# Kernel tuning notes

Hardware: AMD Instinct MI355X
Metric: run time of the kernel (lower is better)

The kernel has to match this reference:

```python
import jax, jax.numpy as jnp
import numpy as np

M, N, NNZ, NITER = 1_000_000, 1_000_000, 8_000_000, 5


def setup_inputs() -> dict:
    key = jax.random.key(0)
    ks = jax.random.split(key, 24)
    f32 = jnp.float32
    inp = dict(
        rows=jax.random.randint(ks[0], (NNZ,), 0, M, dtype=jnp.int32),
        cols=jax.random.randint(ks[1], (NNZ,), 0, N, dtype=jnp.int32),
        vals=jax.random.normal(ks[2], (NNZ,), dtype=f32) * 0.1,
        b=jax.random.normal(ks[3], (M, 1), dtype=f32),
        c=jax.random.normal(ks[4], (N, 1), dtype=f32),
        solution=jax.random.normal(ks[5], (N, 1), dtype=f32),
        dual_solution=jax.random.normal(ks[6], (M, 1), dtype=f32),
        x0=jax.random.normal(ks[7], (N, 1), dtype=f32),  # beta=1 init
        y0=jax.random.normal(ks[8], (M, 1), dtype=f32),  # std_y=1 init
        # dual tower: Conv1d(10->4), Conv1d(6->4), update Conv1d(6->1)
        dw1=jax.random.normal(ks[9], (4, 10), dtype=f32) * 0.3,
        db1=jax.random.normal(ks[10], (4,), dtype=f32) * 0.1,
        dw2=jax.random.normal(ks[11], (4, 6), dtype=f32) * 0.3,
        db2=jax.random.normal(ks[12], (4,), dtype=f32) * 0.1,
        dwu=jax.random.normal(ks[13], (1, 6), dtype=f32) * 0.1,
        dbu=jax.random.normal(ks[14], (1,), dtype=f32) * 0.1,
        # primal tower: Conv1d(10->4), Conv1d(6->4), update Conv1d(6->1)
        pw1=jax.random.normal(ks[15], (4, 10), dtype=f32) * 0.3,
        pb1=jax.random.normal(ks[16], (4,), dtype=f32) * 0.1,
        pw2=jax.random.normal(ks[17], (4, 6), dtype=f32) * 0.3,
        pb2=jax.random.normal(ks[18], (4,), dtype=f32) * 0.1,
        pwu=jax.random.normal(ks[19], (1, 6), dtype=f32) * 0.1,
        pbu=jax.random.normal(ks[20], (1,), dtype=f32) * 0.1,
        nb_max_iter=NITER,
    )
    return inp


def reference(rows, cols, vals, b, c, solution, dual_solution, x0, y0,
              dw1, db1, dw2, db2, dwu, dbu,
              pw1, pb1, pw2, pb2, pwu, pbu, nb_max_iter):
    m, n = b.shape[0], c.shape[0]

    def A_mm(X):   # sparse A @ X : [n,k] -> [m,k]
        return jax.ops.segment_sum(vals[:, None] * X[cols], rows, num_segments=m)

    def At_mm(Y):  # sparse A.T @ Y : [m,k] -> [n,k]
        return jax.ops.segment_sum(vals[:, None] * Y[rows], cols, num_segments=n)

    def step(carry, _):
        x, y, x_h, y_h = carry  # x[n,1] y[m,1] x_h[4,n] y_h[4,m]
        # dual update
        r = A_mm(x) - b                                   # [m,1]
        atxh = A_mm(x_h.T)                                # [m,4]
        h = jnp.concatenate([y_h, atxh.T, y.T, r.T], 0)   # [10,m]
        h = jax.nn.relu(dw1 @ h + db1[:, None])           # [4,m]
        h = jnp.concatenate([h, y.T, r.T], 0)             # [6,m]
        y_h = jax.nn.relu(dw2 @ h + db2[:, None])         # [4,m]
        h2 = jnp.concatenate([y_h, y.T, r.T], 0)          # [6,m]
        y = y + (dwu @ h2 + dbu[:, None]).T               # [m,1]
        # primal update
        d = c + At_mm(y)                                  # [n,1]
        atyh = At_mm(y_h.T)                               # [n,4]
        g = jnp.concatenate([x_h, atyh.T, x.T, d.T], 0)   # [10,n]
        g = jax.nn.relu(pw1 @ g + pb1[:, None])           # [4,n]
        g = jnp.concatenate([g, x.T, d.T], 0)             # [6,n]
        x_h = jax.nn.relu(pw2 @ g + pb2[:, None])         # [4,n]
        g2 = jnp.concatenate([x_h, x.T, d.T], 0)          # [6,n]
        x = x + (pwu @ g2 + pbu[:, None]).T               # [n,1]
        dp = jnp.sqrt(jnp.sum((x - solution) ** 2))
        dd = jnp.sqrt(jnp.sum((y - dual_solution) ** 2))
        return (x, y, x_h, y_h), (dp, dd)

    init = (x0, y0,
            jnp.zeros((4, n), dtype=x0.dtype),
            jnp.zeros((4, m), dtype=y0.dtype))
    (x, y, _, _), (dps, dds) = jax.lax.scan(step, init, None, length=nb_max_iter)

    loss_primal = jnp.mean(dps) + 1.0 * jnp.mean(jax.nn.relu(dps[1:] - dps[:-1]))
    loss_dual = jnp.mean(dds) + 1.0 * jnp.mean(jax.nn.relu(dds[1:] - dds[:-1]))
    loss = loss_primal + loss_dual
    return x, y, loss, dps, dds
```

## Files before the change

kernel.cpp:

```cpp
#include <hip/hip_runtime.h>
#include <math.h>


#define NITER 5
#define NBK_SHIFT 9
#define NBK (1 << NBK_SHIFT)
#define NBK_MAX 2048
#define CH 16384
#define SORT_CAP 6144

__device__ __forceinline__ float blockReduceSum(float v) {
#pragma unroll
  for (int off = 32; off > 0; off >>= 1) v += __shfl_down(v, off, 64);
  __shared__ float smem[8];
  const int lane = threadIdx.x & 63;
  const int wid = threadIdx.x >> 6;
  if (lane == 0) smem[wid] = v;
  __syncthreads();
  float r = 0.f;
  if (threadIdx.x == 0) {
    const int nw = (blockDim.x + 63) >> 6;
    for (int w = 0; w < nw; ++w) r += smem[w];
  }
  return r;
}

__global__ __launch_bounds__(1024) void zero_meta(int* __restrict__ cntA,
                                                  int* __restrict__ cntT,
                                                  float* __restrict__ red) {
  const int i = threadIdx.x;
  cntA[i] = 0;
  cntA[i + 1024] = 0;
  cntT[i] = 0;
  cntT[i + 1024] = 0;
  if (i < 16) red[i] = 0.f;
}

__global__ __launch_bounds__(256) void hist2(const int* __restrict__ rows,
                                             const int* __restrict__ cols,
                                             int* __restrict__ cntA,
                                             int* __restrict__ cntT, int nnz) {
  __shared__ int hA[NBK_MAX];
  __shared__ int hT[NBK_MAX];
  for (int i = threadIdx.x; i < NBK_MAX; i += 256) { hA[i] = 0; hT[i] = 0; }
  __syncthreads();
  const int stride = gridDim.x * blockDim.x;
  for (int e = blockIdx.x * blockDim.x + threadIdx.x; e < nnz; e += stride) {
    atomicAdd(&hA[rows[e] >> NBK_SHIFT], 1);
    atomicAdd(&hT[cols[e] >> NBK_SHIFT], 1);
  }
  __syncthreads();
  for (int i = threadIdx.x; i < NBK_MAX; i += 256) {
    if (hA[i]) atomicAdd(&cntA[i], hA[i]);
    if (hT[i]) atomicAdd(&cntT[i], hT[i]);
  }
}

__global__ __launch_bounds__(1024) void scan_bases(const int* __restrict__ cnt,
                                                   int* __restrict__ base,
                                                   int* __restrict__ fill,
                                                   int nb) {
  __shared__ int sm[1024];
  int run = 0;
  for (int s = 0; s < nb; s += 1024) {
    const int i = s + threadIdx.x;
    const int x = (i < nb) ? cnt[i] : 0;
    sm[threadIdx.x] = x;
    __syncthreads();
#pragma unroll
    for (int off = 1; off < 1024; off <<= 1) {
      const int add = (threadIdx.x >= off) ? sm[threadIdx.x - off] : 0;
      __syncthreads();
      sm[threadIdx.x] += add;
      __syncthreads();
    }
    if (i < nb) {
      const int ex = run + sm[threadIdx.x] - x;
      base[i] = ex;
      fill[i] = ex;
    }
    const int tot = sm[1023];
    __syncthreads();
    run += tot;
  }
}

__global__ __launch_bounds__(512) void scatter2(
    const int* __restrict__ rows, const int* __restrict__ cols,
    const float* __restrict__ vals, int* __restrict__ fillA,
    int* __restrict__ fillT, int2* __restrict__ eA, int2* __restrict__ eT,
    int nnz) {
  __shared__ int hA[NBK_MAX];
  __shared__ int hT[NBK_MAX];
  for (int i = threadIdx.x; i < NBK_MAX; i += 512) { hA[i] = 0; hT[i] = 0; }
  __syncthreads();
  const int e0 = blockIdx.x * CH;
  for (int k = threadIdx.x; k < CH; k += 512) {
    const int e = e0 + k;
    if (e < nnz) {
      atomicAdd(&hA[rows[e] >> NBK_SHIFT], 1);
      atomicAdd(&hT[cols[e] >> NBK_SHIFT], 1);
    }
  }
  __syncthreads();
  for (int i = threadIdx.x; i < NBK_MAX; i += 512) {
    const int cA = hA[i];
    if (cA) hA[i] = atomicAdd(&fillA[i], cA);
    const int cT = hT[i];
    if (cT) hT[i] = atomicAdd(&fillT[i], cT);
  }
  __syncthreads();
  for (int k = threadIdx.x; k < CH; k += 512) {
    const int e = e0 + k;
    if (e < nnz) {
      const int r = rows[e];
      const int c = cols[e];
      const int vb = __float_as_int(vals[e]);
      const int pA = atomicAdd(&hA[r >> NBK_SHIFT], 1);
      eA[pA] = make_int2(((r & (NBK - 1)) << 20) | c, vb);
      const int pT = atomicAdd(&hT[c >> NBK_SHIFT], 1);
      eT[pT] = make_int2(((c & (NBK - 1)) << 20) | r, vb);
    }
  }
}

__global__ __launch_bounds__(512) void sort_bucket(const int* __restrict__ base,
                                                   const int* __restrict__ cnt,
                                                   int2* __restrict__ edges) {
  __shared__ int2 recs[SORT_CAP];
  __shared__ int hist[NBK];
  const int bkt = blockIdx.x;
  const int beg = base[bkt];
  const int num = cnt[bkt];
  if (num > SORT_CAP) return;
  if (threadIdx.x < NBK) hist[threadIdx.x] = 0;
  __syncthreads();
  for (int k = threadIdx.x; k < num; k += 512) {
    const int2 r = edges[beg + k];
    recs[k] = r;
    atomicAdd(&hist[((unsigned)r.x) >> 20], 1);
  }
  __syncthreads();
  int x = 0, incl = 0;
  if (threadIdx.x < NBK) { x = hist[threadIdx.x]; incl = x; }
#pragma unroll
  for (int off = 1; off < NBK; off <<= 1) {
    int add = 0;
    if (threadIdx.x < NBK && threadIdx.x >= off) add = hist[threadIdx.x - off];
    __syncthreads();
    if (threadIdx.x < NBK) {
      incl += add;
      hist[threadIdx.x] = incl;
    }
    __syncthreads();
  }
  if (threadIdx.x < NBK) hist[threadIdx.x] = incl - x;
  __syncthreads();
  for (int k = threadIdx.x; k < num; k += 512) {
    const int2 r = recs[k];
    const int p = atomicAdd(&hist[((unsigned)r.x) >> 20], 1);
    edges[beg + p] = r;
  }
}

__global__ __launch_bounds__(256) void init_state2(const float* __restrict__ x0,
                                                   const float* __restrict__ y0,
                                                   float* __restrict__ X5,
                                                   float* __restrict__ Y5,
                                                   int n, int m) {
  const int i = blockIdx.x * blockDim.x + threadIdx.x;
  if (i < n) {
    float* xp = X5 + (size_t)i * 8;
    xp[0] = x0[i];
    xp[1] = 0.f; xp[2] = 0.f; xp[3] = 0.f; xp[4] = 0.f;
  }
  if (i < m) {
    float* yp = Y5 + (size_t)i * 8;
    yp[0] = y0[i];
    yp[1] = 0.f; yp[2] = 0.f; yp[3] = 0.f; yp[4] = 0.f;
  }
}

__global__ __launch_bounds__(256) void fused_bucket_tower(
    const int* __restrict__ base, const int* __restrict__ cnt,
    const int2* __restrict__ edges, const float* __restrict__ src,
    float* __restrict__ state, const float* __restrict__ seed, float sign,
    const float* __restrict__ sol, const float* __restrict__ w1,
    const float* __restrict__ b1, const float* __restrict__ w2,
    const float* __restrict__ b2, const float* __restrict__ wu,
    const float* __restrict__ bu, float* __restrict__ red_slot, int count) {
  __shared__ float acc[NBK * 5];
  for (int i = threadIdx.x; i < NBK * 5; i += 256) acc[i] = 0.f;
  __syncthreads();
  const int bkt = blockIdx.x;
  const int beg = base[bkt];
  const int num = cnt[bkt];
  const int lane = threadIdx.x & 63;
  for (int k0 = 0; k0 < num; k0 += 512) {
    const int kA = k0 + threadIdx.x;
    const int kB = k0 + 256 + threadIdx.x;
    int dlA = -1, dlB = -1;
    float vA = 0.f, vB = 0.f;
    float4 loA = make_float4(0.f, 0.f, 0.f, 0.f);
    float4 loB = make_float4(0.f, 0.f, 0.f, 0.f);
    float s4A = 0.f, s4B = 0.f;
    if (kA < num) {
      const int2 ed = edges[beg + kA];
      dlA = ((unsigned)ed.x) >> 20;
      vA = __int_as_float(ed.y);
      const float* sp = src + (size_t)(ed.x & 0xFFFFF) * 8;
      loA = *reinterpret_cast<const float4*>(sp);
      s4A = sp[4];
    }
    if (kB < num) {
      const int2 ed = edges[beg + kB];
      dlB = ((unsigned)ed.x) >> 20;
      vB = __int_as_float(ed.y);
      const float* sp = src + (size_t)(ed.x & 0xFFFFF) * 8;
      loB = *reinterpret_cast<const float4*>(sp);
      s4B = sp[4];
    }
    {
      float m0 = vA * loA.x, m1 = vA * loA.y, m2 = vA * loA.z,
            m3 = vA * loA.w, m4 = vA * s4A;
      int dl = dlA;
#pragma unroll
      for (int off = 1; off < 64; off <<= 1) {
        const int dlu = __shfl_up(dl, off, 64);
        const float t0 = __shfl_up(m0, off, 64);
        const float t1 = __shfl_up(m1, off, 64);
        const float t2 = __shfl_up(m2, off, 64);
        const float t3 = __shfl_up(m3, off, 64);
        const float t4 = __shfl_up(m4, off, 64);
        if (lane >= off && dlu == dl) {
          m0 += t0; m1 += t1; m2 += t2; m3 += t3; m4 += t4;
        }
      }
      const int dld = __shfl_down(dl, 1, 64);
      if (dl >= 0 && ((lane == 63) || (dld != dl))) {
        float* ap = acc + dl * 5;
        atomicAdd(ap + 0, m0);
        atomicAdd(ap + 1, m1);
        atomicAdd(ap + 2, m2);
        atomicAdd(ap + 3, m3);
        atomicAdd(ap + 4, m4);
      }
    }
    {
      float m0 = vB * loB.x, m1 = vB * loB.y, m2 = vB * loB.z,
            m3 = vB * loB.w, m4 = vB * s4B;
      int dl = dlB;
#pragma unroll
      for (int off = 1; off < 64; off <<= 1) {
        const int dlu = __shfl_up(dl, off, 64);
        const float t0 = __shfl_up(m0, off, 64);
        const float t1 = __shfl_up(m1, off, 64);
        const float t2 = __shfl_up(m2, off, 64);
        const float t3 = __shfl_up(m3, off, 64);
        const float t4 = __shfl_up(m4, off, 64);
        if (lane >= off && dlu == dl) {
          m0 += t0; m1 += t1; m2 += t2; m3 += t3; m4 += t4;
        }
      }
      const int dld = __shfl_down(dl, 1, 64);
      if (dl >= 0 && ((lane == 63) || (dld != dl))) {
        float* ap = acc + dl * 5;
        atomicAdd(ap + 0, m0);
        atomicAdd(ap + 1, m1);
        atomicAdd(ap + 2, m2);
        atomicAdd(ap + 3, m3);
        atomicAdd(ap + 4, m4);
      }
    }
  }
  __syncthreads();
  float part = 0.f;
  for (int t = threadIdx.x; t < NBK; t += 256) {
    const int row = (bkt << NBK_SHIFT) + t;
    if (row < count) {
      const float* a = acc + t * 5;
      const float r = a[0] + sign * seed[row];
      float* sp = state + (size_t)row * 8;
      const float4 st = *reinterpret_cast<const float4*>(sp);
      const float y = st.x;
      float v[10];
      v[0] = st.y; v[1] = st.z; v[2] = st.w; v[3] = sp[4];
      v[4] = a[1]; v[5] = a[2]; v[6] = a[3]; v[7] = a[4];
      v[8] = y;
      v[9] = r;
      float h[4];
#pragma unroll
      for (int o = 0; o < 4; ++o) {
        float accv = b1[o];
#pragma unroll
        for (int kk = 0; kk < 10; ++kk) accv += w1[o * 10 + kk] * v[kk];
        h[o] = fmaxf(accv, 0.f);
      }
      float hn[4];
#pragma unroll
      for (int o = 0; o < 4; ++o) {
        float accv = b2[o] + w2[o * 6 + 4] * y + w2[o * 6 + 5] * r;
#pragma unroll
        for (int kk = 0; kk < 4; ++kk) accv += w2[o * 6 + kk] * h[kk];
        hn[o] = fmaxf(accv, 0.f);
      }
      const float upd = bu[0] + wu[0] * hn[0] + wu[1] * hn[1] + wu[2] * hn[2] +
                        wu[3] * hn[3] + wu[4] * y + wu[5] * r;
      const float yn = y + upd;
      float4 stn;
      stn.x = yn; stn.y = hn[0]; stn.z = hn[1]; stn.w = hn[2];
      *reinterpret_cast<float4*>(sp) = stn;
      sp[4] = hn[3];
      const float diff = yn - sol[row];
      part += diff * diff;
    }
  }
  const float bs = blockReduceSum(part);
  if (threadIdx.x == 0) unsafeAtomicAdd(red_slot, bs);
}

__global__ __launch_bounds__(256) void finalize2(const float* __restrict__ X5,
                                                 const float* __restrict__ Y5,
                                                 const float* __restrict__ red,
                                                 float* __restrict__ out, int n,
                                                 int m) {
  const int i = blockIdx.x * blockDim.x + threadIdx.x;
  if (i < n) out[i] = X5[(size_t)i * 8];
  if (i < m) out[n + i] = Y5[(size_t)i * 8];
  if (i == 0) {
    float dps[NITER], dds[NITER];
#pragma unroll
    for (int t = 0; t < NITER; ++t) {
      dps[t] = sqrtf(red[t]);
      dds[t] = sqrtf(red[NITER + t]);
    }
    float mp = 0.f, md = 0.f, rp = 0.f, rd = 0.f;
#pragma unroll
    for (int t = 0; t < NITER; ++t) { mp += dps[t]; md += dds[t]; }
#pragma unroll
    for (int t = 1; t < NITER; ++t) {
      rp += fmaxf(dps[t] - dps[t - 1], 0.f);
      rd += fmaxf(dds[t] - dds[t - 1], 0.f);
    }
    out[n + m] = mp / NITER + rp / (NITER - 1) + md / NITER + rd / (NITER - 1);
#pragma unroll
    for (int t = 0; t < NITER; ++t) {
      out[n + m + 1 + t] = dps[t];
      out[n + m + 1 + NITER + t] = dds[t];
    }
  }
}

template <int S>
__global__ __launch_bounds__(256) void init_state(
    const float* __restrict__ x0, const float* __restrict__ y0,
    const float* __restrict__ b, float* __restrict__ X5,
    float* __restrict__ Y5, float* __restrict__ Yacc, float* __restrict__ red,
    int n, int m) {
  const int i = blockIdx.x * blockDim.x + threadIdx.x;
  if (i < 16) red[i] = 0.f;
  if (i < n) {
    float* xp = X5 + (size_t)i * S;
    xp[0] = x0[i];
    xp[1] = 0.f; xp[2] = 0.f; xp[3] = 0.f; xp[4] = 0.f;
  }
  if (i < m) {
    float* yp = Y5 + (size_t)i * S;
    yp[0] = y0[i];
    yp[1] = 0.f; yp[2] = 0.f; yp[3] = 0.f; yp[4] = 0.f;
    float* ya = Yacc + (size_t)i * S;
    ya[0] = -b[i];
    ya[1] = 0.f; ya[2] = 0.f; ya[3] = 0.f; ya[4] = 0.f;
  }
}

template <int S>
__global__ __launch_bounds__(256) void spmm5(const int* __restrict__ gidx,
                                             const int* __restrict__ sidx,
                                             const float* __restrict__ vals,
                                             const float* __restrict__ src,
                                             float* __restrict__ dst, int nnz) {
  const int e = blockIdx.x * blockDim.x + threadIdx.x;
  if (e >= nnz) return;
  const int g = gidx[e];
  const int s = sidx[e];
  const float v = vals[e];
  const float* sp = src + (size_t)g * S;
  float s0, s1, s2, s3, s4;
  if constexpr (S == 8) {
    const float4 lo = *reinterpret_cast<const float4*>(sp);
    s0 = lo.x; s1 = lo.y; s2 = lo.z; s3 = lo.w; s4 = sp[4];
  } else {
    s0 = sp[0]; s1 = sp[1]; s2 = sp[2]; s3 = sp[3]; s4 = sp[4];
  }
  float* dp = dst + (size_t)s * S;
  unsafeAtomicAdd(dp + 0, v * s0);
  unsafeAtomicAdd(dp + 1, v * s1);
  unsafeAtomicAdd(dp + 2, v * s2);
  unsafeAtomicAdd(dp + 3, v * s3);
  unsafeAtomicAdd(dp + 4, v * s4);
}

template <int S>
__global__ __launch_bounds__(256) void tower(
    const float* __restrict__ acc, float* __restrict__ state,
    const float* __restrict__ prep_src, float* __restrict__ prep_dst,
    float sign, const float* __restrict__ sol, const float* __restrict__ w1,
    const float* __restrict__ b1, const float* __restrict__ w2,
    const float* __restrict__ b2, const float* __restrict__ wu,
    const float* __restrict__ bu, float* __restrict__ red_slot, int count,
    int prep_count) {
  const int i = blockIdx.x * blockDim.x + threadIdx.x;
  float part = 0.f;
  if (i < count) {
    const float* a = acc + (size_t)i * S;
    const float r = a[0];
    float* sp = state + (size_t)i * S;
    const float y = sp[0];
    float v[10];
    v[0] = sp[1]; v[1] = sp[2]; v[2] = sp[3]; v[3] = sp[4];
    v[4] = a[1];  v[5] = a[2];  v[6] = a[3];  v[7] = a[4];
    v[8] = y;
    v[9] = r;
    float h[4];
#pragma unroll
    for (int o = 0; o < 4; ++o) {
      float accv = b1[o];
#pragma unroll
      for (int k = 0; k < 10; ++k) accv += w1[o * 10 + k] * v[k];
      h[o] = fmaxf(accv, 0.f);
    }
    float hn[4];
#pragma unroll
    for (int o = 0; o < 4; ++o) {
      float accv = b2[o] + w2[o * 6 + 4] * y + w2[o * 6 + 5] * r;
#pragma unroll
      for (int k = 0; k < 4; ++k) accv += w2[o * 6 + k] * h[k];
      hn[o] = fmaxf(accv, 0.f);
    }
    const float upd = bu[0] + wu[0] * hn[0] + wu[1] * hn[1] + wu[2] * hn[2] +
                      wu[3] * hn[3] + wu[4] * y + wu[5] * r;
    const float yn = y + upd;
    sp[0] = yn;
    sp[1] = hn[0]; sp[2] = hn[1]; sp[3] = hn[2]; sp[4] = hn[3];
    const float diff = yn - sol[i];
    part = diff * diff;
  }
  if (i < prep_count) {
    float* pd = prep_dst + (size_t)i * S;
    pd[0] = sign * prep_src[i];
    pd[1] = 0.f; pd[2] = 0.f; pd[3] = 0.f; pd[4] = 0.f;
  }
  const float bs = blockReduceSum(part);
  if (threadIdx.x == 0) unsafeAtomicAdd(red_slot, bs);
}

template <int S>
static void run_atomic(const int* rows, const int* cols, const float* vals,
                       const float* b, const float* c, const float* solution,
                       const float* dual_solution, const float* x0,
                       const float* y0, const float* dw1, const float* db1,
                       const float* dw2, const float* db2, const float* dwu,
                       const float* dbu, const float* pw1, const float* pb1,
                       const float* pw2, const float* pb2, const float* pwu,
                       const float* pbu, float* out, float* ws, int n, int m,
                       int nnz, hipStream_t stream) {
  float* X5 = ws;
  float* Y5 = X5 + (size_t)n * S;
  float* Xacc = Y5 + (size_t)m * S;
  float* Yacc = Xacc + (size_t)n * S;
  float* red = Yacc + (size_t)m * S;

  const int BLK = 256;
  const int nm = (n > m) ? n : m;
  const int gN = (nm + BLK - 1) / BLK;
  const int gE = (nnz + BLK - 1) / BLK;

  init_state<S><<<gN, BLK, 0, stream>>>(x0, y0, b, X5, Y5, Yacc, red, n, m);
  for (int t = 0; t < NITER; ++t) {
    spmm5<S><<<gE, BLK, 0, stream>>>(cols, rows, vals, X5, Yacc, nnz);
    tower<S><<<gN, BLK, 0, stream>>>(Yacc, Y5, c, Xacc, 1.0f, dual_solution,
                                     dw1, db1, dw2, db2, dwu, dbu,
                                     red + NITER + t, m, n);
    spmm5<S><<<gE, BLK, 0, stream>>>(rows, cols, vals, Y5, Xacc, nnz);
    tower<S><<<gN, BLK, 0, stream>>>(Xacc, X5, b, Yacc, -1.0f, solution, pw1,
                                     pb1, pw2, pb2, pwu, pbu, red + t, n, m);
  }
  finalize2<<<gN, BLK, 0, stream>>>(X5, Y5, red, out, n, m);
}

static inline size_t alignUp(size_t x, size_t a) { return (x + a - 1) / a * a; }

extern "C" void kernel_launch(void* const* d_in, const int* in_sizes, int n_in,
                              void* d_out, int out_size, void* d_ws,
                              size_t ws_size, hipStream_t stream) {
  const int* rows = (const int*)d_in[0];
  const int* cols = (const int*)d_in[1];
  const float* vals = (const float*)d_in[2];
  const float* b = (const float*)d_in[3];
  const float* c = (const float*)d_in[4];
  const float* solution = (const float*)d_in[5];
  const float* dual_solution = (const float*)d_in[6];
  const float* x0 = (const float*)d_in[7];
  const float* y0 = (const float*)d_in[8];
  const float* dw1 = (const float*)d_in[9];
  const float* db1 = (const float*)d_in[10];
  const float* dw2 = (const float*)d_in[11];
  const float* db2 = (const float*)d_in[12];
  const float* dwu = (const float*)d_in[13];
  const float* dbu = (const float*)d_in[14];
  const float* pw1 = (const float*)d_in[15];
  const float* pb1 = (const float*)d_in[16];
  const float* pw2 = (const float*)d_in[17];
  const float* pb2 = (const float*)d_in[18];
  const float* pwu = (const float*)d_in[19];
  const float* pbu = (const float*)d_in[20];

  const int nnz = in_sizes[0];
  const int m = in_sizes[3];
  const int n = in_sizes[4];
  float* out = (float*)d_out;
  char* ws = (char*)d_ws;

  const int nbA = (m + NBK - 1) >> NBK_SHIFT;
  const int nbT = (n + NBK - 1) >> NBK_SHIFT;

  size_t off = 0;
  const size_t oX5 = off;    off = alignUp(off + (size_t)n * 8 * 4, 256);
  const size_t oY5 = off;    off = alignUp(off + (size_t)m * 8 * 4, 256);
  const size_t oEA = off;    off = alignUp(off + (size_t)nnz * 8, 256);
  const size_t oET = off;    off = alignUp(off + (size_t)nnz * 8, 256);
  const size_t oCntA = off;  off = alignUp(off + (size_t)NBK_MAX * 4, 256);
  const size_t oBasA = off;  off = alignUp(off + (size_t)NBK_MAX * 4, 256);
  const size_t oFilA = off;  off = alignUp(off + (size_t)NBK_MAX * 4, 256);
  const size_t oCntT = off;  off = alignUp(off + (size_t)NBK_MAX * 4, 256);
  const size_t oBasT = off;  off = alignUp(off + (size_t)NBK_MAX * 4, 256);
  const size_t oFilT = off;  off = alignUp(off + (size_t)NBK_MAX * 4, 256);
  const size_t oRed = off;   off = alignUp(off + 16 * 4, 256);
  const size_t needB = off;

  const bool ok = (nbA <= NBK_MAX) && (nbT <= NBK_MAX) && (m <= (1 << 20)) &&
                  (n <= (1 << 20)) && (ws_size >= needB);

  if (ok) {
    float* X5 = (float*)(ws + oX5);
    float* Y5 = (float*)(ws + oY5);
    int2* eA = (int2*)(ws + oEA);
    int2* eT = (int2*)(ws + oET);
    int* cntA = (int*)(ws + oCntA);
    int* basA = (int*)(ws + oBasA);
    int* filA = (int*)(ws + oFilA);
    int* cntT = (int*)(ws + oCntT);
    int* basT = (int*)(ws + oBasT);
    int* filT = (int*)(ws + oFilT);
    float* red = (float*)(ws + oRed);

    const int BLK = 256;
    const int nm = (n > m) ? n : m;
    const int gN = (nm + BLK - 1) / BLK;
    const int gC = (nnz + CH - 1) / CH;

    zero_meta<<<1, 1024, 0, stream>>>(cntA, cntT, red);
    hist2<<<512, BLK, 0, stream>>>(rows, cols, cntA, cntT, nnz);
    scan_bases<<<1, 1024, 0, stream>>>(cntA, basA, filA, nbA);
    scan_bases<<<1, 1024, 0, stream>>>(cntT, basT, filT, nbT);
    scatter2<<<gC, 512, 0, stream>>>(rows, cols, vals, filA, filT, eA, eT,
                                     nnz);
    sort_bucket<<<nbA, 512, 0, stream>>>(basA, cntA, eA);
    sort_bucket<<<nbT, 512, 0, stream>>>(basT, cntT, eT);
    init_state2<<<gN, BLK, 0, stream>>>(x0, y0, X5, Y5, n, m);

    for (int t = 0; t < NITER; ++t) {
      fused_bucket_tower<<<nbA, BLK, 0, stream>>>(
          basA, cntA, eA, X5, Y5, b, -1.0f, dual_solution, dw1, db1, dw2, db2,
          dwu, dbu, red + NITER + t, m);
      fused_bucket_tower<<<nbT, BLK, 0, stream>>>(
          basT, cntT, eT, Y5, X5, c, 1.0f, solution, pw1, pb1, pw2, pb2, pwu,
          pbu, red + t, n);
    }
    finalize2<<<gN, BLK, 0, stream>>>(X5, Y5, red, out, n, m);
    return;
  }

  const size_t need8 =
      ((size_t)n * 8 + (size_t)m * 8) * 2 * sizeof(float) + 64 * sizeof(float);
  if (ws_size >= need8) {
    run_atomic<8>(rows, cols, vals, b, c, solution, dual_solution, x0, y0, dw1,
                  db1, dw2, db2, dwu, dbu, pw1, pb1, pw2, pb2, pwu, pbu, out,
                  (float*)d_ws, n, m, nnz, stream);
  } else {
    run_atomic<5>(rows, cols, vals, b, c, solution, dual_solution, x0, y0, dw1,
                  db1, dw2, db2, dwu, dbu, pw1, pb1, pw2, pb2, pwu, pbu, out,
                  (float*)d_ws, n, m, nnz, stream);
  }
}
```

Measured before the change: 2.267 ms.

## Vectorize histogram loads, nontemporal edge stores, and deepen gather unroll in tower

The histogram passes in hist2 and scatter2 now read rows and cols as int4 vectors. Edge records in scatter2 are written with nontemporal 64-bit stores, and the sort bucket capacity grows so more buckets fit in shared memory. The sort kernel drops its thread guards, which are redundant because NBK equals the block size. The fused tower now issues four independent edge gathers per iteration instead of two to expose more memory-level parallelism, at the cost of more registers.

```diff
diff --git a/kernel.cpp b/kernel.cpp
--- a/kernel.cpp
+++ b/kernel.cpp
@@ -7,7 +7,7 @@
 #define NBK (1 << NBK_SHIFT)
 #define NBK_MAX 2048
 #define CH 16384
-#define SORT_CAP 6144
+#define SORT_CAP 7168
 
 __device__ __forceinline__ float blockReduceSum(float v) {
 #pragma unroll
@@ -44,8 +44,24 @@
   __shared__ int hT[NBK_MAX];
   for (int i = threadIdx.x; i < NBK_MAX; i += 256) { hA[i] = 0; hT[i] = 0; }
   __syncthreads();
+  const int gid = blockIdx.x * blockDim.x + threadIdx.x;
   const int stride = gridDim.x * blockDim.x;
-  for (int e = blockIdx.x * blockDim.x + threadIdx.x; e < nnz; e += stride) {
+  const int n4 = nnz >> 2;
+  const int4* r4 = (const int4*)rows;
+  const int4* c4 = (const int4*)cols;
+  for (int e = gid; e < n4; e += stride) {
+    const int4 r = r4[e];
+    const int4 c = c4[e];
+    atomicAdd(&hA[r.x >> NBK_SHIFT], 1);
+    atomicAdd(&hA[r.y >> NBK_SHIFT], 1);
+    atomicAdd(&hA[r.z >> NBK_SHIFT], 1);
+    atomicAdd(&hA[r.w >> NBK_SHIFT], 1);
+    atomicAdd(&hT[c.x >> NBK_SHIFT], 1);
+    atomicAdd(&hT[c.y >> NBK_SHIFT], 1);
+    atomicAdd(&hT[c.z >> NBK_SHIFT], 1);
+    atomicAdd(&hT[c.w >> NBK_SHIFT], 1);
+  }
+  for (int e = (n4 << 2) + gid; e < nnz; e += stride) {
     atomicAdd(&hA[rows[e] >> NBK_SHIFT], 1);
     atomicAdd(&hT[cols[e] >> NBK_SHIFT], 1);
   }
@@ -95,11 +111,28 @@
   for (int i = threadIdx.x; i < NBK_MAX; i += 512) { hA[i] = 0; hT[i] = 0; }
   __syncthreads();
   const int e0 = blockIdx.x * CH;
-  for (int k = threadIdx.x; k < CH; k += 512) {
-    const int e = e0 + k;
-    if (e < nnz) {
-      atomicAdd(&hA[rows[e] >> NBK_SHIFT], 1);
-      atomicAdd(&hT[cols[e] >> NBK_SHIFT], 1);
+  if (e0 + CH <= nnz) {
+    const int4* r4 = (const int4*)(rows + e0);
+    const int4* c4 = (const int4*)(cols + e0);
+    for (int k = threadIdx.x; k < (CH >> 2); k += 512) {
+      const int4 r = r4[k];
+      const int4 c = c4[k];
+      atomicAdd(&hA[r.x >> NBK_SHIFT], 1);
+      atomicAdd(&hA[r.y >> NBK_SHIFT], 1);
+      atomicAdd(&hA[r.z >> NBK_SHIFT], 1);
+      atomicAdd(&hA[r.w >> NBK_SHIFT], 1);
+      atomicAdd(&hT[c.x >> NBK_SHIFT], 1);
+      atomicAdd(&hT[c.y >> NBK_SHIFT], 1);
+      atomicAdd(&hT[c.z >> NBK_SHIFT], 1);
+      atomicAdd(&hT[c.w >> NBK_SHIFT], 1);
+    }
+  } else {
+    for (int k = threadIdx.x; k < CH; k += 512) {
+      const int e = e0 + k;
+      if (e < nnz) {
+        atomicAdd(&hA[rows[e] >> NBK_SHIFT], 1);
+        atomicAdd(&hT[cols[e] >> NBK_SHIFT], 1);
+      }
     }
   }
   __syncthreads();
@@ -115,11 +148,15 @@
     if (e < nnz) {
       const int r = rows[e];
       const int c = cols[e];
-      const int vb = __float_as_int(vals[e]);
+      const unsigned vb = (unsigned)__float_as_int(vals[e]);
       const int pA = atomicAdd(&hA[r >> NBK_SHIFT], 1);
-      eA[pA] = make_int2(((r & (NBK - 1)) << 20) | c, vb);
+      const unsigned long long recA =
+          (unsigned)(((r & (NBK - 1)) << 20) | c) | ((unsigned long long)vb << 32);
+      __builtin_nontemporal_store(recA, (unsigned long long*)eA + pA);
       const int pT = atomicAdd(&hT[c >> NBK_SHIFT], 1);
-      eT[pT] = make_int2(((c & (NBK - 1)) << 20) | r, vb);
+      const unsigned long long recT =
+          (unsigned)(((c & (NBK - 1)) << 20) | r) | ((unsigned long long)vb << 32);
+      __builtin_nontemporal_store(recT, (unsigned long long*)eT + pT);
     }
   }
 }
@@ -133,7 +170,7 @@
   const int beg = base[bkt];
   const int num = cnt[bkt];
   if (num > SORT_CAP) return;
-  if (threadIdx.x < NBK) hist[threadIdx.x] = 0;
+  hist[threadIdx.x] = 0;
   __syncthreads();
   for (int k = threadIdx.x; k < num; k += 512) {
     const int2 r = edges[beg + k];
@@ -141,20 +178,18 @@
     atomicAdd(&hist[((unsigned)r.x) >> 20], 1);
   }
   __syncthreads();
-  int x = 0, incl = 0;
-  if (threadIdx.x < NBK) { x = hist[threadIdx.x]; incl = x; }
+  const int x = hist[threadIdx.x];
+  int incl = x;
 #pragma unroll
   for (int off = 1; off < NBK; off <<= 1) {
     int add = 0;
-    if (threadIdx.x < NBK && threadIdx.x >= off) add = hist[threadIdx.x - off];
+    if (threadIdx.x >= off) add = hist[threadIdx.x - off];
     __syncthreads();
-    if (threadIdx.x < NBK) {
-      incl += add;
-      hist[threadIdx.x] = incl;
-    }
+    incl += add;
+    hist[threadIdx.x] = incl;
     __syncthreads();
   }
-  if (threadIdx.x < NBK) hist[threadIdx.x] = incl - x;
+  hist[threadIdx.x] = incl - x;
   __syncthreads();
   for (int k = threadIdx.x; k < num; k += 512) {
     const int2 r = recs[k];
@@ -181,6 +216,32 @@
   }
 }
 
+__device__ __forceinline__ void segscan_flush(int dl, float m0, float m1,
+                                              float m2, float m3, float m4,
+                                              int lane, float* __restrict__ acc) {
+#pragma unroll
+  for (int off = 1; off < 64; off <<= 1) {
+    const int dlu = __shfl_up(dl, off, 64);
+    const float t0 = __shfl_up(m0, off, 64);
+    const float t1 = __shfl_up(m1, off, 64);
+    const float t2 = __shfl_up(m2, off, 64);
+    const float t3 = __shfl_up(m3, off, 64);
+    const float t4 = __shfl_up(m4, off, 64);
+    if (lane >= off && dlu == dl) {
+      m0 += t0; m1 += t1; m2 += t2; m3 += t3; m4 += t4;
+    }
+  }
+  const int dld = __shfl_down(dl, 1, 64);
+  if (dl >= 0 && ((lane == 63) || (dld != dl))) {
+    float* ap = acc + dl * 5;
+    atomicAdd(ap + 0, m0);
+    atomicAdd(ap + 1, m1);
+    atomicAdd(ap + 2, m2);
+    atomicAdd(ap + 3, m3);
+    atomicAdd(ap + 4, m4);
+  }
+}
+
 __global__ __launch_bounds__(256) void fused_bucket_tower(
     const int* __restrict__ base, const int* __restrict__ cnt,
     const int2* __restrict__ edges, const float* __restrict__ src,
@@ -196,82 +257,56 @@
   const int beg = base[bkt];
   const int num = cnt[bkt];
   const int lane = threadIdx.x & 63;
-  for (int k0 = 0; k0 < num; k0 += 512) {
+  for (int k0 = 0; k0 < num; k0 += 1024) {
     const int kA = k0 + threadIdx.x;
-    const int kB = k0 + 256 + threadIdx.x;
-    int dlA = -1, dlB = -1;
-    float vA = 0.f, vB = 0.f;
-    float4 loA = make_float4(0.f, 0.f, 0.f, 0.f);
-    float4 loB = make_float4(0.f, 0.f, 0.f, 0.f);
-    float s4A = 0.f, s4B = 0.f;
+    const int kB = kA + 256;
+    const int kC = kA + 512;
+    const int kD = kA + 768;
+    int dA = -1, dB = -1, dC = -1, dD = -1;
+    float vA = 0.f, vB = 0.f, vC = 0.f, vD = 0.f;
+    float4 lA = make_float4(0.f, 0.f, 0.f, 0.f);
+    float4 lB = lA, lC = lA, lD = lA;
+    float sA = 0.f, sB = 0.f, sC = 0.f, sD = 0.f;
     if (kA < num) {
-      const int2 ed = edges[beg + kA];
-      dlA = ((unsigned)ed.x) >> 20;
-      vA = __int_as_float(ed.y);
-      const float* sp = src + (size_t)(ed.x & 0xFFFFF) * 8;
-      loA = *reinterpret_cast<const float4*>(sp);
-      s4A = sp[4];
+      const int2 e = edges[beg + kA];
+      dA = ((unsigned)e.x) >> 20;
+      vA = __int_as_float(e.y);
+      const float* sp = src + (size_t)(e.x & 0xFFFFF) * 8;
+      lA = *reinterpret_cast<const float4*>(sp);
+      sA = sp[4];
     }
     if (kB < num) {
-      const int2 ed = edges[beg + kB];
-      dlB = ((unsigned)ed.x) >> 20;
-      vB = __int_as_float(ed.y);
-      const float* sp = src + (size_t)(ed.x & 0xFFFFF) * 8;
-      loB = *reinterpret_cast<const float4*>(sp);
-      s4B = sp[4];
-    }
-    {
-      float m0 = vA * loA.x, m1 = vA * loA.y, m2 = vA * loA.z,
-            m3 = vA * loA.w, m4 = vA * s4A;
-      int dl = dlA;
-#pragma unroll
-      for (int off = 1; off < 64; off <<= 1) {
-        const int dlu = __shfl_up(dl, off, 64);
-        const float t0 = __shfl_up(m0, off, 64);
-        const float t1 = __shfl_up(m1, off, 64);
-        const float t2 = __shfl_up(m2, off, 64);
-        const float t3 = __shfl_up(m3, off, 64);
-        const float t4 = __shfl_up(m4, off, 64);
-        if (lane >= off && dlu == dl) {
-          m0 += t0; m1 += t1; m2 += t2; m3 += t3; m4 += t4;
-        }
-      }
-      const int dld = __shfl_down(dl, 1, 64);
-      if (dl >= 0 && ((lane == 63) || (dld != dl))) {
-        float* ap = acc + dl * 5;
-        atomicAdd(ap + 0, m0);
-        atomicAdd(ap + 1, m1);
-        atomicAdd(ap + 2, m2);
-        atomicAdd(ap + 3, m3);
-        atomicAdd(ap + 4, m4);
-      }
-    }
-    {
-      float m0 = vB * loB.x, m1 = vB * loB.y, m2 = vB * loB.z,
-            m3 = vB * loB.w, m4 = vB * s4B;
-      int dl = dlB;
-#pragma unroll
-      for (int off = 1; off < 64; off <<= 1) {
-        const int dlu = __shfl_up(dl, off, 64);
-        const float t0 = __shfl_up(m0, off, 64);
-        const float t1 = __shfl_up(m1, off, 64);
-        const float t2 = __shfl_up(m2, off, 64);
-        const float t3 = __shfl_up(m3, off, 64);
-        const float t4 = __shfl_up(m4, off, 64);
-        if (lane >= off && dlu == dl) {
-          m0 += t0; m1 += t1; m2 += t2; m3 += t3; m4 += t4;
-        }
-      }
-      const int dld = __shfl_down(dl, 1, 64);
-      if (dl >= 0 && ((lane == 63) || (dld != dl))) {
-        float* ap = acc + dl * 5;
-        atomicAdd(ap + 0, m0);
-        atomicAdd(ap + 1, m1);
-        atomicAdd(ap + 2, m2);
-        atomicAdd(ap + 3, m3);
-        atomicAdd(ap + 4, m4);
-      }
-    }
+      const int2 e = edges[beg + kB];
+      dB = ((unsigned)e.x) >> 20;
+      vB = __int_as_float(e.y);
+      const float* sp = src + (size_t)(e.x & 0xFFFFF) * 8;
+      lB = *reinterpret_cast<const float4*>(sp);
+      sB = sp[4];
+    }
+    if (kC < num) {
+      const int2 e = edges[beg + kC];
+      dC = ((unsigned)e.x) >> 20;
+      vC = __int_as_float(e.y);
+      const float* sp = src + (size_t)(e.x & 0xFFFFF) * 8;
+      lC = *reinterpret_cast<const float4*>(sp);
+      sC = sp[4];
+    }
+    if (kD < num) {
+      const int2 e = edges[beg + kD];
+      dD = ((unsigned)e.x) >> 20;
+      vD = __int_as_float(e.y);
+      const float* sp = src + (size_t)(e.x & 0xFFFFF) * 8;
+      lD = *reinterpret_cast<const float4*>(sp);
+      sD = sp[4];
+    }
+    segscan_flush(dA, vA * lA.x, vA * lA.y, vA * lA.z, vA * lA.w, vA * sA,
+                  lane, acc);
+    segscan_flush(dB, vB * lB.x, vB * lB.y, vB * lB.z, vB * lB.w, vB * sB,
+                  lane, acc);
+    segscan_flush(dC, vC * lC.x, vC * lC.y, vC * lC.z, vC * lC.w, vC * sC,
+                  lane, acc);
+    segscan_flush(dD, vD * lD.x, vD * lD.y, vD * lD.z, vD * lD.w, vD * sD,
+                  lane, acc);
   }
   __syncthreads();
   float part = 0.f;
```

Measured after the change: 2.677 ms. +18.1%, slower.
